# Performance work log

Hardware: AMD Instinct MI355X
Metric: run time of the kernel (lower is better)

The kernel has to match this reference:

```python
import jax, jax.numpy as jnp
import numpy as np

TEMP = 0.1
QUEUE_SIZE = 512
CUTOFF_KM = 25.0
EARTH_R_KM = 6371.0088


def _normalize(x, eps=1e-12):
    # F.normalize: x / max(||x||, eps)
    n = jnp.linalg.norm(x, axis=-1, keepdims=True)
    return x / jnp.maximum(n, eps)


def _haversine_km(g1, g2):
    # g1: (B,2) [lat,lon] degrees; g2: (S,2) -> (B,S) great-circle km
    r = jnp.pi / 180.0
    lat1 = g1[:, 0:1] * r
    lon1 = g1[:, 1:2] * r
    lat2 = g2[None, :, 0] * r
    lon2 = g2[None, :, 1] * r
    dlat = lat2 - lat1
    dlon = lon2 - lon1
    a = jnp.sin(dlat / 2) ** 2 + jnp.cos(lat1) * jnp.cos(lat2) * jnp.sin(dlon / 2) ** 2
    return 2.0 * EARTH_R_KM * jnp.arcsin(jnp.sqrt(jnp.clip(a, 0.0, 1.0)))


def setup_inputs() -> dict:
    key = jax.random.key(0)
    k = jax.random.split(key, 7)
    n_aug, B, D, S = 4, 256, 768, 65536
    V = jax.random.normal(k[0], (n_aug, B, D), jnp.float32)
    L = jax.random.normal(k[1], (B, D), jnp.float32)
    gps = jnp.concatenate([
        jax.random.uniform(k[2], (B, 1), jnp.float32, -90.0, 90.0),
        jax.random.uniform(k[3], (B, 1), jnp.float32, -180.0, 180.0)], axis=1)
    support_features = jax.random.normal(k[4], (S, D), jnp.float32)
    support_gps = jnp.concatenate([
        jax.random.uniform(k[5], (S, 1), jnp.float32, -90.0, 90.0),
        jax.random.uniform(k[6], (S, 1), jnp.float32, -180.0, 180.0)], axis=1)
    return {"V": V, "L": L, "gps": gps,
            "support_features": support_features, "support_gps": support_gps}


def reference(V, L, gps, support_features, support_gps):
    # org joint embedding always from V[0]; nearest neighbour over raw support feats
    org = _normalize(V[0] * L)                                   # (B,D)
    sim = org @ support_features.T                               # (B,S)
    nn_idx = jnp.argmax(sim, axis=1)                             # (B,)
    nn = _normalize(support_features[nn_idx])                    # (B,D)

    # augmented joints for j = 1..n_aug-1
    augs = _normalize(V[1:] * L[None])                           # (J,B,D)
    # numerator always uses V[1] (as in the original code), constant over j
    num = jnp.einsum('bd,bd->b', nn, augs[0]) / TEMP             # (B,)

    # in-batch denominator: sum_i exp(nn_b . aug_{j,i} / T)
    batch_den = jnp.exp(jnp.einsum('bd,jid->jbi', nn, augs) / TEMP).sum(axis=2)  # (J,B)

    # GPS-filtered negative queue: first QUEUE_SIZE support entries > 25 km away,
    # zero-padded (zero rows contribute exp(0) = 1, matching the torch code)
    mask = _haversine_km(gps, support_gps) > CUTOFF_KM           # (B,S)
    order = jnp.argsort(jnp.where(mask, 0, 1), axis=1)[:, :QUEUE_SIZE]  # stable: kept in original order
    valid = jnp.take_along_axis(mask, order, axis=1)             # (B,Q)
    qfeat = support_features[order] * valid[..., None]           # (B,Q,D)
    queue_den = jnp.exp(jnp.einsum('bd,bqd->bq', nn, qfeat) / TEMP).sum(axis=1)  # (B,)

    den = jnp.log(batch_den + queue_den[None, :])                # (J,B)
    loss = -(num[None, :] - den).sum() / V.shape[1]
    return loss
```

## Files before the change

### kernel.cpp

```cpp
#include <hip/hip_runtime.h>
#include <hip/hip_bf16.h>

#define B_ROWS 256
#define S_SUP  65536
#define D_DIM  768
#define QSZ    512
#define NCHUNK 12
#define CHUNK_BYTES 32768

typedef short bf16x8 __attribute__((ext_vector_type(8)));
typedef float f32x4  __attribute__((ext_vector_type(4)));

__device__ __forceinline__ bf16x8 cvt8(float4 a, float4 b) {
  bf16x8 r;
  r[0] = (short)(__float_as_uint(a.x) >> 16);
  r[1] = (short)(__float_as_uint(a.y) >> 16);
  r[2] = (short)(__float_as_uint(a.z) >> 16);
  r[3] = (short)(__float_as_uint(a.w) >> 16);
  r[4] = (short)(__float_as_uint(b.x) >> 16);
  r[5] = (short)(__float_as_uint(b.y) >> 16);
  r[6] = (short)(__float_as_uint(b.z) >> 16);
  r[7] = (short)(__float_as_uint(b.w) >> 16);
  return r;
}

__device__ __forceinline__ void gl_lds16(const void* g, void* l) {
  __builtin_amdgcn_global_load_lds(
      (const __attribute__((address_space(1))) unsigned int*)g,
      (__attribute__((address_space(3))) unsigned int*)l, 16, 0, 0);
}

__device__ __forceinline__ float block_sum(float v) {
  __shared__ float tmp[4];
  #pragma unroll
  for (int m = 32; m >= 1; m >>= 1) v += __shfl_xor(v, m, 64);
  __syncthreads();
  if ((threadIdx.x & 63) == 0) tmp[threadIdx.x >> 6] = v;
  __syncthreads();
  return tmp[0] + tmp[1] + tmp[2] + tmp[3];
}

__device__ __forceinline__ double block_sum_d(double v) {
  __shared__ double tmp[4];
  #pragma unroll
  for (int m = 32; m >= 1; m >>= 1) v += __shfl_xor(v, m, 64);
  __syncthreads();
  if ((threadIdx.x & 63) == 0) tmp[threadIdx.x >> 6] = v;
  __syncthreads();
  return tmp[0] + tmp[1] + tmp[2] + tmp[3];
}

__global__ __launch_bounds__(256) void init_kernel(unsigned long long* gmax, double* bden) {
  int t = threadIdx.x;
  gmax[t] = 0ull;
  for (int i = t; i < 3 * B_ROWS; i += 256) bden[i] = 0.0;
}

__global__ __launch_bounds__(256) void prep_kernel(const float* __restrict__ V,
                                                   const float* __restrict__ L,
                                                   unsigned short* __restrict__ orgb,
                                                   float* __restrict__ augs) {
  int jb = blockIdx.x;
  int j = jb >> 8, b = jb & 255;
  int tid = threadIdx.x;
  const float* v = V + ((size_t)j * B_ROWS + b) * D_DIM;
  const float* l = L + (size_t)b * D_DIM;
  float p[3]; float ssq = 0.f;
  #pragma unroll
  for (int i = 0; i < 3; ++i) {
    int k = tid + 256 * i;
    p[i] = v[k] * l[k];
    ssq += p[i] * p[i];
  }
  ssq = block_sum(ssq);
  float inv = 1.0f / fmaxf(sqrtf(ssq), 1e-12f);
  if (j == 0) {
    #pragma unroll
    for (int i = 0; i < 3; ++i) {
      int k = tid + 256 * i;
      unsigned short hv = (unsigned short)(__float_as_uint(p[i] * inv) >> 16);
      int c = k >> 6, kk = k & 63, jg = kk >> 3, e = kk & 7;
      orgb[c * 16384 + b * 64 + ((jg ^ (b & 7)) << 3) + e] = hv;
    }
  } else {
    float* dst = augs + ((size_t)(j - 1) * B_ROWS + b) * D_DIM;
    #pragma unroll
    for (int i = 0; i < 3; ++i) dst[tid + 256 * i] = p[i] * inv;
  }
}

__global__ __launch_bounds__(256) void sim_argmax_kernel(const unsigned short* __restrict__ orgb,
                                                         const float* __restrict__ sf,
                                                         unsigned long long* __restrict__ gmax) {
  const int tid  = threadIdx.x;
  const int w    = tid >> 6;
  const int lid  = tid & 63;
  const int quad = lid >> 4;
  const int r15  = lid & 15;
  const int s_col = blockIdx.x * 64 + w * 16 + r15;

  __shared__ __align__(16) char smem[CHUNK_BYTES];

  f32x4 acc[16];
  #pragma unroll
  for (int t = 0; t < 16; ++t) acc[t] = (f32x4){0.f, 0.f, 0.f, 0.f};

  const float* bp = sf + (size_t)s_col * D_DIM + quad * 8;
  const char* gsrc_base = (const char*)orgb;

  for (int c = 0; c < NCHUNK; ++c) {
    {
      const char* g = gsrc_base + c * CHUNK_BYTES + w * 8192 + lid * 16;
      char* ldst = smem + w * 8192;
      #pragma unroll
      for (int i = 0; i < 8; ++i)
        gl_lds16(g + i * 1024, ldst + i * 1024);
    }
    __syncthreads();

    #pragma unroll
    for (int k1 = 0; k1 < 2; ++k1) {
      int k0 = c * 64 + k1 * 32;
      float4 b0 = *(const float4*)(bp + k0);
      float4 b1 = *(const float4*)(bp + k0 + 4);
      bf16x8 bf = cvt8(b0, b1);
      int abase = r15 * 128 + (((k1 * 4 + quad) ^ (r15 & 7)) << 4);
      #pragma unroll
      for (int t = 0; t < 16; ++t) {
        bf16x8 af = *(const bf16x8*)(smem + abase + t * 2048);
        acc[t] = __builtin_amdgcn_mfma_f32_16x16x32_bf16(af, bf, acc[t], 0, 0, 0);
      }
    }
    __syncthreads();
  }

  __shared__ float smax[4 * 256];
  __shared__ int   sidx[4 * 256];
  #pragma unroll
  for (int t = 0; t < 16; ++t) {
    #pragma unroll
    for (int r = 0; r < 4; ++r) {
      float v = acc[t][r];
      int   idx = s_col;
      #pragma unroll
      for (int m = 1; m < 16; m <<= 1) {
        float ov = __shfl_xor(v, m, 64);
        int   oi = __shfl_xor(idx, m, 64);
        if (ov > v || (ov == v && oi < idx)) { v = ov; idx = oi; }
      }
      if (r15 == 0) {
        int b = 16 * t + 4 * quad + r;
        smax[w * 256 + b] = v;
        sidx[w * 256 + b] = idx;
      }
    }
  }
  __syncthreads();
  {
    int b = tid;
    float v = smax[b]; int idx = sidx[b];
    #pragma unroll
    for (int w2 = 1; w2 < 4; ++w2) {
      float ov = smax[w2 * 256 + b]; int oi = sidx[w2 * 256 + b];
      if (ov > v || (ov == v && oi < idx)) { v = ov; idx = oi; }
    }
    unsigned u = __float_as_uint(v);
    unsigned key = (u & 0x80000000u) ? ~u : (u | 0x80000000u);
    unsigned long long packed = ((unsigned long long)key << 32) |
                                (unsigned long long)(0xFFFFFFFFu - (unsigned)idx);
    atomicMax(gmax + b, packed);
  }
}

__global__ __launch_bounds__(256) void nn_kernel(const unsigned long long* __restrict__ gmax,
                                                 const float* __restrict__ sf,
                                                 const float* __restrict__ augs,
                                                 float* __restrict__ nn,
                                                 float* __restrict__ nnT,
                                                 float* __restrict__ num) {
  int b = blockIdx.x, tid = threadIdx.x;
  int idx = (int)(0xFFFFFFFFu - (unsigned)(gmax[b] & 0xFFFFFFFFull));
  const float* row = sf + (size_t)idx * D_DIM;
  float p[3]; float ssq = 0.f;
  #pragma unroll
  for (int i = 0; i < 3; ++i) { p[i] = row[tid + 256 * i]; ssq += p[i] * p[i]; }
  ssq = block_sum(ssq);
  float inv = 1.0f / fmaxf(sqrtf(ssq), 1e-12f);
  const float* a0 = augs + (size_t)b * D_DIM;
  float dot = 0.f;
  #pragma unroll
  for (int i = 0; i < 3; ++i) {
    int k = tid + 256 * i;
    float nv = p[i] * inv;
    nn[(size_t)b * D_DIM + k] = nv;
    nnT[(size_t)k * B_ROWS + b] = nv;
    dot += nv * a0[k];
  }
  dot = block_sum(dot);
  if (tid == 0) num[b] = dot * 10.0f;
}

__global__ __launch_bounds__(256) void bden_kernel(const float* __restrict__ augs,
                                                   const float* __restrict__ nnT,
                                                   double* __restrict__ bden) {
  int jc = blockIdx.x;
  int j = jc >> 6, c = jc & 63;
  int i0 = c * 4;
  __shared__ float s_aug[4 * D_DIM];
  const float* src = augs + ((size_t)j * B_ROWS + i0) * D_DIM;
  for (int idx = threadIdx.x; idx < 4 * D_DIM; idx += 256) s_aug[idx] = src[idx];
  __syncthreads();
  int b = threadIdx.x;
  float a0 = 0.f, a1 = 0.f, a2 = 0.f, a3 = 0.f;
  for (int k = 0; k < D_DIM; ++k) {
    float nv = nnT[(size_t)k * B_ROWS + b];
    a0 += nv * s_aug[k];
    a1 += nv * s_aug[D_DIM + k];
    a2 += nv * s_aug[2 * D_DIM + k];
    a3 += nv * s_aug[3 * D_DIM + k];
  }
  double v = exp((double)a0 * 10.0) + exp((double)a1 * 10.0) +
             exp((double)a2 * 10.0) + exp((double)a3 * 10.0);
  atomicAdd(&bden[j * B_ROWS + b], v);
}

__global__ __launch_bounds__(256) void queue_kernel(const float* __restrict__ gps,
                                                    const float* __restrict__ sgps,
                                                    const float* __restrict__ sf,
                                                    const float* __restrict__ nn,
                                                    double* __restrict__ qden) {
  int b = blockIdx.x, tid = threadIdx.x;
  int w = tid >> 6, lane = tid & 63;
  __shared__ int qidx[QSZ];
  __shared__ int s_count;
  __shared__ int s_wcnt[4];
  __shared__ __align__(16) float s_nn[D_DIM];
  __shared__ double s_gsum[16];
  for (int k = tid; k < D_DIM; k += 256) s_nn[k] = nn[(size_t)b * D_DIM + k];
  if (tid == 0) s_count = 0;
  __syncthreads();

  const float r = 0.017453292519943295f;
  float lat1 = gps[b * 2 + 0] * r, lon1 = gps[b * 2 + 1] * r;
  float cl1 = cosf(lat1);
  int base = 0;
  while (true) {
    int count = s_count;
    if (count >= QSZ || base >= S_SUP) break;
    int s = base + tid;
    float lat2 = sgps[s * 2 + 0] * r, lon2 = sgps[s * 2 + 1] * r;
    float sdlat = sinf((lat2 - lat1) * 0.5f);
    float sdlon = sinf((lon2 - lon1) * 0.5f);
    float a = sdlat * sdlat + cl1 * cosf(lat2) * sdlon * sdlon;
    a = fminf(fmaxf(a, 0.f), 1.f);
    float d = 2.0f * 6371.0088f * asinf(sqrtf(a));
    bool valid = d > 25.0f;

    unsigned long long m = __ballot(valid);
    int wc = __popcll(m);
    if (lane == 0) s_wcnt[w] = wc;
    __syncthreads();
    int wbase = count;
    for (int i = 0; i < w; ++i) wbase += s_wcnt[i];
    int pos = wbase + __popcll(m & ((1ull << lane) - 1ull));
    if (valid && pos < QSZ) qidx[pos] = s;
    __syncthreads();
    if (tid == 0) {
      int total = s_wcnt[0] + s_wcnt[1] + s_wcnt[2] + s_wcnt[3];
      s_count = min(QSZ, count + total);
    }
    base += 256;
    __syncthreads();
  }
  int count = s_count;

  int g  = lane >> 4;
  int l2 = lane & 15;
  double acc = 0.0;
  const float4* nn4 = (const float4*)s_nn;
  for (int q = w * 4 + g; q < count; q += 16) {
    const float4* row = (const float4*)(sf + (size_t)qidx[q] * D_DIM);
    float dot = 0.f;
    #pragma unroll
    for (int i = 0; i < 12; ++i) {
      float4 a = row[l2 + 16 * i];
      float4 nv = nn4[l2 + 16 * i];
      dot += a.x * nv.x + a.y * nv.y + a.z * nv.z + a.w * nv.w;
    }
    #pragma unroll
    for (int m2 = 8; m2 >= 1; m2 >>= 1) dot += __shfl_xor(dot, m2, 16);
    if (l2 == 0) acc += exp((double)dot * 10.0);
  }
  if (l2 == 0) s_gsum[w * 4 + g] = acc;
  __syncthreads();
  if (tid == 0) {
    double t = (double)(QSZ - count);
    #pragma unroll
    for (int i = 0; i < 16; ++i) t += s_gsum[i];
    qden[b] = t;
  }
}

__global__ __launch_bounds__(256) void loss_kernel(const float* __restrict__ num,
                                                   const double* __restrict__ bden,
                                                   const double* __restrict__ qden,
                                                   float* __restrict__ out) {
  int b = threadIdx.x;
  double q = qden[b];
  double n = (double)num[b];
  double t = 0.0;
  #pragma unroll
  for (int j = 0; j < 3; ++j) t += n - log(bden[j * B_ROWS + b] + q);
  t = block_sum_d(t);
  if (b == 0) out[0] = (float)(-t / 256.0);
}

extern "C" void kernel_launch(void* const* d_in, const int* in_sizes, int n_in,
                              void* d_out, int out_size, void* d_ws, size_t ws_size,
                              hipStream_t stream) {
  const float* V    = (const float*)d_in[0];
  const float* L    = (const float*)d_in[1];
  const float* gps  = (const float*)d_in[2];
  const float* sf   = (const float*)d_in[3];
  const float* sgps = (const float*)d_in[4];
  float* out = (float*)d_out;

  char* ws = (char*)d_ws;
  size_t off = 0;
  unsigned short* orgb = (unsigned short*)(ws + off); off += 393216;
  float* augs = (float*)(ws + off); off += 2359296;
  float* nn   = (float*)(ws + off); off += 786432;
  float* nnT  = (float*)(ws + off); off += 786432;
  float* num  = (float*)(ws + off); off += 1024;
  double* bden = (double*)(ws + off); off += 6144;
  double* qden = (double*)(ws + off); off += 2048;
  unsigned long long* gmax = (unsigned long long*)(ws + off); off += 2048;

  init_kernel<<<1, 256, 0, stream>>>(gmax, bden);
  prep_kernel<<<1024, 256, 0, stream>>>(V, L, orgb, augs);
  sim_argmax_kernel<<<S_SUP / 64, 256, 0, stream>>>(orgb, sf, gmax);
  nn_kernel<<<B_ROWS, 256, 0, stream>>>(gmax, sf, augs, nn, nnT, num);
  bden_kernel<<<192, 256, 0, stream>>>(augs, nnT, bden);
  queue_kernel<<<B_ROWS, 256, 0, stream>>>(gps, sgps, sf, nn, qden);
  loss_kernel<<<1, 256, 0, stream>>>(num, bden, qden, out);
}
```

Measured before the change: 432.3 us.

## Double-buffer sim GEMM with LDS-staged B tiles and fuse small kernels

Restructures the similarity/argmax kernel. Each wave now computes a 64x64 register tile (4x4 MFMA tiles) instead of 16x256. The support-feature B operand is converted to bf16 once into LDS and shared across waves, and A and B chunks are double-buffered so the next loads overlap the current MFMAs. The argmax epilogue does atomicMax per row directly, dropping the shared-memory cross-wave reduction. It also folds the init work into prep_kernel and merges nn_kernel with queue_kernel, which removes the intermediate nn buffer and two launches, at the cost of more LDS per block and more atomics.

```diff
diff --git a/kernel.cpp b/kernel.cpp
--- a/kernel.cpp
+++ b/kernel.cpp
@@ -6,7 +6,8 @@
 #define D_DIM  768
 #define QSZ    512
 #define NCHUNK 12
-#define CHUNK_BYTES 32768
+#define ACH_BYTES 32768
+#define BCH_BYTES 8192
 
 typedef short bf16x8 __attribute__((ext_vector_type(8)));
 typedef float f32x4  __attribute__((ext_vector_type(4)));
@@ -50,19 +51,19 @@
   return tmp[0] + tmp[1] + tmp[2] + tmp[3];
 }
 
-__global__ __launch_bounds__(256) void init_kernel(unsigned long long* gmax, double* bden) {
-  int t = threadIdx.x;
-  gmax[t] = 0ull;
-  for (int i = t; i < 3 * B_ROWS; i += 256) bden[i] = 0.0;
-}
-
 __global__ __launch_bounds__(256) void prep_kernel(const float* __restrict__ V,
                                                    const float* __restrict__ L,
                                                    unsigned short* __restrict__ orgb,
-                                                   float* __restrict__ augs) {
+                                                   float* __restrict__ augs,
+                                                   unsigned long long* __restrict__ gmax,
+                                                   double* __restrict__ bden) {
   int jb = blockIdx.x;
   int j = jb >> 8, b = jb & 255;
   int tid = threadIdx.x;
+  if (jb == 0) {
+    gmax[tid] = 0ull;
+    for (int i = tid; i < 3 * B_ROWS; i += 256) bden[i] = 0.0;
+  }
   const float* v = V + ((size_t)j * B_ROWS + b) * D_DIM;
   const float* l = L + (size_t)b * D_DIM;
   float p[3]; float ssq = 0.f;
@@ -89,59 +90,90 @@
   }
 }
 
-__global__ __launch_bounds__(256) void sim_argmax_kernel(const unsigned short* __restrict__ orgb,
-                                                         const float* __restrict__ sf,
-                                                         unsigned long long* __restrict__ gmax) {
+__global__ __launch_bounds__(256, 2) void sim_argmax_kernel(const unsigned short* __restrict__ orgb,
+                                                            const float* __restrict__ sf,
+                                                            unsigned long long* __restrict__ gmax) {
   const int tid  = threadIdx.x;
   const int w    = tid >> 6;
   const int lid  = tid & 63;
   const int quad = lid >> 4;
   const int r15  = lid & 15;
-  const int s_col = blockIdx.x * 64 + w * 16 + r15;
-
-  __shared__ __align__(16) char smem[CHUNK_BYTES];
-
-  f32x4 acc[16];
-  #pragma unroll
-  for (int t = 0; t < 16; ++t) acc[t] = (f32x4){0.f, 0.f, 0.f, 0.f};
-
-  const float* bp = sf + (size_t)s_col * D_DIM + quad * 8;
-  const char* gsrc_base = (const char*)orgb;
+  const int s0   = blockIdx.x * 64;
+
+  __shared__ __align__(16) char bufA[2][ACH_BYTES];
+  __shared__ __align__(16) char bufB[2][BCH_BYTES];
+
+  f32x4 acc[4][4];
+  #pragma unroll
+  for (int mt = 0; mt < 4; ++mt)
+    #pragma unroll
+    for (int nt = 0; nt < 4; ++nt) acc[mt][nt] = (f32x4){0.f, 0.f, 0.f, 0.f};
+
+  const float* bsrc = sf + (size_t)(s0 + lid) * D_DIM + w * 16;
+  const char*  asrc = (const char*)orgb;
+  const int lrow = lid * 128;
+  const int sl0  = (((2 * w)     ^ (lid & 7)) << 4);
+  const int sl1  = (((2 * w + 1) ^ (lid & 7)) << 4);
+
+  {
+    const char* g = asrc + w * 8192 + lid * 16;
+    char* l = bufA[0] + w * 8192;
+    #pragma unroll
+    for (int i = 0; i < 8; ++i) gl_lds16(g + i * 1024, l + i * 1024);
+    const float4* bp = (const float4*)bsrc;
+    float4 q0 = bp[0], q1 = bp[1], q2 = bp[2], q3 = bp[3];
+    *(bf16x8*)(bufB[0] + lrow + sl0) = cvt8(q0, q1);
+    *(bf16x8*)(bufB[0] + lrow + sl1) = cvt8(q2, q3);
+  }
+  __syncthreads();
 
   for (int c = 0; c < NCHUNK; ++c) {
-    {
-      const char* g = gsrc_base + c * CHUNK_BYTES + w * 8192 + lid * 16;
-      char* ldst = smem + w * 8192;
-      #pragma unroll
-      for (int i = 0; i < 8; ++i)
-        gl_lds16(g + i * 1024, ldst + i * 1024);
-    }
-    __syncthreads();
-
+    float4 q0, q1, q2, q3;
+    const int nb = (c + 1) & 1;
+    if (c < NCHUNK - 1) {
+      const char* g = asrc + (c + 1) * ACH_BYTES + w * 8192 + lid * 16;
+      char* l = bufA[nb] + w * 8192;
+      #pragma unroll
+      for (int i = 0; i < 8; ++i) gl_lds16(g + i * 1024, l + i * 1024);
+      const float4* bp = (const float4*)(bsrc + (c + 1) * 64);
+      q0 = bp[0]; q1 = bp[1]; q2 = bp[2]; q3 = bp[3];
+    }
+    const char* Ac = bufA[c & 1];
+    const char* Bc = bufB[c & 1];
     #pragma unroll
     for (int k1 = 0; k1 < 2; ++k1) {
-      int k0 = c * 64 + k1 * 32;
-      float4 b0 = *(const float4*)(bp + k0);
-      float4 b1 = *(const float4*)(bp + k0 + 4);
-      bf16x8 bf = cvt8(b0, b1);
-      int abase = r15 * 128 + (((k1 * 4 + quad) ^ (r15 & 7)) << 4);
-      #pragma unroll
-      for (int t = 0; t < 16; ++t) {
-        bf16x8 af = *(const bf16x8*)(smem + abase + t * 2048);
-        acc[t] = __builtin_amdgcn_mfma_f32_16x16x32_bf16(af, bf, acc[t], 0, 0, 0);
+      const int slot = (((k1 * 4 + quad) ^ (r15 & 7)) << 4);
+      bf16x8 af[4], bfr[4];
+      #pragma unroll
+      for (int mt = 0; mt < 4; ++mt)
+        af[mt] = *(const bf16x8*)(Ac + (64 * w + 16 * mt + r15) * 128 + slot);
+      #pragma unroll
+      for (int nt = 0; nt < 4; ++nt)
+        bfr[nt] = *(const bf16x8*)(Bc + (16 * nt + r15) * 128 + slot);
+      #pragma unroll
+      for (int mt = 0; mt < 4; ++mt)
+        #pragma unroll
+        for (int nt = 0; nt < 4; ++nt)
+          acc[mt][nt] = __builtin_amdgcn_mfma_f32_16x16x32_bf16(af[mt], bfr[nt], acc[mt][nt], 0, 0, 0);
+    }
+    if (c < NCHUNK - 1) {
+      *(bf16x8*)(bufB[nb] + lrow + sl0) = cvt8(q0, q1);
+      *(bf16x8*)(bufB[nb] + lrow + sl1) = cvt8(q2, q3);
+      __syncthreads();
+    }
+  }
+
+  #pragma unroll
+  for (int mt = 0; mt < 4; ++mt) {
+    #pragma unroll
+    for (int r = 0; r < 4; ++r) {
+      float v = acc[mt][0][r];
+      int idx = s0 + r15;
+      #pragma unroll
+      for (int nt = 1; nt < 4; ++nt) {
+        float c2 = acc[mt][nt][r];
+        if (c2 > v) { v = c2; idx = s0 + nt * 16 + r15; }
       }
-    }
-    __syncthreads();
-  }
-
-  __shared__ float smax[4 * 256];
-  __shared__ int   sidx[4 * 256];
-  #pragma unroll
-  for (int t = 0; t < 16; ++t) {
-    #pragma unroll
-    for (int r = 0; r < 4; ++r) {
-      float v = acc[t][r];
-      int   idx = s_col;
       #pragma unroll
       for (int m = 1; m < 16; m <<= 1) {
         float ov = __shfl_xor(v, m, 64);
@@ -149,36 +181,33 @@
         if (ov > v || (ov == v && oi < idx)) { v = ov; idx = oi; }
       }
       if (r15 == 0) {
-        int b = 16 * t + 4 * quad + r;
-        smax[w * 256 + b] = v;
-        sidx[w * 256 + b] = idx;
+        int mg = 64 * w + 16 * mt + 4 * quad + r;
+        unsigned u = __float_as_uint(v);
+        unsigned key = (u & 0x80000000u) ? ~u : (u | 0x80000000u);
+        unsigned long long packed = ((unsigned long long)key << 32) |
+                                    (unsigned long long)(0xFFFFFFFFu - (unsigned)idx);
+        atomicMax(gmax + mg, packed);
       }
     }
   }
-  __syncthreads();
-  {
-    int b = tid;
-    float v = smax[b]; int idx = sidx[b];
-    #pragma unroll
-    for (int w2 = 1; w2 < 4; ++w2) {
-      float ov = smax[w2 * 256 + b]; int oi = sidx[w2 * 256 + b];
-      if (ov > v || (ov == v && oi < idx)) { v = ov; idx = oi; }
-    }
-    unsigned u = __float_as_uint(v);
-    unsigned key = (u & 0x80000000u) ? ~u : (u | 0x80000000u);
-    unsigned long long packed = ((unsigned long long)key << 32) |
-                                (unsigned long long)(0xFFFFFFFFu - (unsigned)idx);
-    atomicMax(gmax + b, packed);
-  }
-}
-
-__global__ __launch_bounds__(256) void nn_kernel(const unsigned long long* __restrict__ gmax,
-                                                 const float* __restrict__ sf,
-                                                 const float* __restrict__ augs,
-                                                 float* __restrict__ nn,
-                                                 float* __restrict__ nnT,
-                                                 float* __restrict__ num) {
+}
+
+__global__ __launch_bounds__(256) void nnqueue_kernel(const unsigned long long* __restrict__ gmax,
+                                                      const float* __restrict__ sf,
+                                                      const float* __restrict__ augs,
+                                                      const float* __restrict__ gps,
+                                                      const float* __restrict__ sgps,
+                                                      float* __restrict__ nnT,
+                                                      float* __restrict__ num,
+                                                      double* __restrict__ qden) {
   int b = blockIdx.x, tid = threadIdx.x;
+  int w = tid >> 6, lane = tid & 63;
+  __shared__ __align__(16) float s_nn[D_DIM];
+  __shared__ int qidx[QSZ];
+  __shared__ int s_count;
+  __shared__ int s_wcnt[4];
+  __shared__ double s_gsum[16];
+
   int idx = (int)(0xFFFFFFFFu - (unsigned)(gmax[b] & 0xFFFFFFFFull));
   const float* row = sf + (size_t)idx * D_DIM;
   float p[3]; float ssq = 0.f;
@@ -192,52 +221,12 @@
   for (int i = 0; i < 3; ++i) {
     int k = tid + 256 * i;
     float nv = p[i] * inv;
-    nn[(size_t)b * D_DIM + k] = nv;
+    s_nn[k] = nv;
     nnT[(size_t)k * B_ROWS + b] = nv;
     dot += nv * a0[k];
   }
   dot = block_sum(dot);
-  if (tid == 0) num[b] = dot * 10.0f;
-}
-
-__global__ __launch_bounds__(256) void bden_kernel(const float* __restrict__ augs,
-                                                   const float* __restrict__ nnT,
-                                                   double* __restrict__ bden) {
-  int jc = blockIdx.x;
-  int j = jc >> 6, c = jc & 63;
-  int i0 = c * 4;
-  __shared__ float s_aug[4 * D_DIM];
-  const float* src = augs + ((size_t)j * B_ROWS + i0) * D_DIM;
-  for (int idx = threadIdx.x; idx < 4 * D_DIM; idx += 256) s_aug[idx] = src[idx];
-  __syncthreads();
-  int b = threadIdx.x;
-  float a0 = 0.f, a1 = 0.f, a2 = 0.f, a3 = 0.f;
-  for (int k = 0; k < D_DIM; ++k) {
-    float nv = nnT[(size_t)k * B_ROWS + b];
-    a0 += nv * s_aug[k];
-    a1 += nv * s_aug[D_DIM + k];
-    a2 += nv * s_aug[2 * D_DIM + k];
-    a3 += nv * s_aug[3 * D_DIM + k];
-  }
-  double v = exp((double)a0 * 10.0) + exp((double)a1 * 10.0) +
-             exp((double)a2 * 10.0) + exp((double)a3 * 10.0);
-  atomicAdd(&bden[j * B_ROWS + b], v);
-}
-
-__global__ __launch_bounds__(256) void queue_kernel(const float* __restrict__ gps,
-                                                    const float* __restrict__ sgps,
-                                                    const float* __restrict__ sf,
-                                                    const float* __restrict__ nn,
-                                                    double* __restrict__ qden) {
-  int b = blockIdx.x, tid = threadIdx.x;
-  int w = tid >> 6, lane = tid & 63;
-  __shared__ int qidx[QSZ];
-  __shared__ int s_count;
-  __shared__ int s_wcnt[4];
-  __shared__ __align__(16) float s_nn[D_DIM];
-  __shared__ double s_gsum[16];
-  for (int k = tid; k < D_DIM; k += 256) s_nn[k] = nn[(size_t)b * D_DIM + k];
-  if (tid == 0) s_count = 0;
+  if (tid == 0) { num[b] = dot * 10.0f; s_count = 0; }
   __syncthreads();
 
   const float r = 0.017453292519943295f;
@@ -279,17 +268,17 @@
   double acc = 0.0;
   const float4* nn4 = (const float4*)s_nn;
   for (int q = w * 4 + g; q < count; q += 16) {
-    const float4* row = (const float4*)(sf + (size_t)qidx[q] * D_DIM);
-    float dot = 0.f;
+    const float4* rr = (const float4*)(sf + (size_t)qidx[q] * D_DIM);
+    float d2 = 0.f;
     #pragma unroll
     for (int i = 0; i < 12; ++i) {
-      float4 a = row[l2 + 16 * i];
+      float4 a = rr[l2 + 16 * i];
       float4 nv = nn4[l2 + 16 * i];
-      dot += a.x * nv.x + a.y * nv.y + a.z * nv.z + a.w * nv.w;
-    }
-    #pragma unroll
-    for (int m2 = 8; m2 >= 1; m2 >>= 1) dot += __shfl_xor(dot, m2, 16);
-    if (l2 == 0) acc += exp((double)dot * 10.0);
+      d2 += a.x * nv.x + a.y * nv.y + a.z * nv.z + a.w * nv.w;
+    }
+    #pragma unroll
+    for (int m2 = 8; m2 >= 1; m2 >>= 1) d2 += __shfl_xor(d2, m2, 16);
+    if (l2 == 0) acc += exp((double)d2 * 10.0);
   }
   if (l2 == 0) s_gsum[w * 4 + g] = acc;
   __syncthreads();
@@ -299,6 +288,30 @@
     for (int i = 0; i < 16; ++i) t += s_gsum[i];
     qden[b] = t;
   }
+}
+
+__global__ __launch_bounds__(256) void bden_kernel(const float* __restrict__ augs,
+                                                   const float* __restrict__ nnT,
+                                                   double* __restrict__ bden) {
+  int jc = blockIdx.x;
+  int j = jc >> 6, c = jc & 63;
+  int i0 = c * 4;
+  __shared__ float s_aug[4 * D_DIM];
+  const float* src = augs + ((size_t)j * B_ROWS + i0) * D_DIM;
+  for (int idx = threadIdx.x; idx < 4 * D_DIM; idx += 256) s_aug[idx] = src[idx];
+  __syncthreads();
+  int b = threadIdx.x;
+  float a0 = 0.f, a1 = 0.f, a2 = 0.f, a3 = 0.f;
+  for (int k = 0; k < D_DIM; ++k) {
+    float nv = nnT[(size_t)k * B_ROWS + b];
+    a0 += nv * s_aug[k];
+    a1 += nv * s_aug[D_DIM + k];
+    a2 += nv * s_aug[2 * D_DIM + k];
+    a3 += nv * s_aug[3 * D_DIM + k];
+  }
+  double v = exp((double)a0 * 10.0) + exp((double)a1 * 10.0) +
+             exp((double)a2 * 10.0) + exp((double)a3 * 10.0);
+  atomicAdd(&bden[j * B_ROWS + b], v);
 }
 
 __global__ __launch_bounds__(256) void loss_kernel(const float* __restrict__ num,
@@ -329,18 +342,15 @@
   size_t off = 0;
   unsigned short* orgb = (unsigned short*)(ws + off); off += 393216;
   float* augs = (float*)(ws + off); off += 2359296;
-  float* nn   = (float*)(ws + off); off += 786432;
   float* nnT  = (float*)(ws + off); off += 786432;
   float* num  = (float*)(ws + off); off += 1024;
   double* bden = (double*)(ws + off); off += 6144;
   double* qden = (double*)(ws + off); off += 2048;
   unsigned long long* gmax = (unsigned long long*)(ws + off); off += 2048;
 
-  init_kernel<<<1, 256, 0, stream>>>(gmax, bden);
-  prep_kernel<<<1024, 256, 0, stream>>>(V, L, orgb, augs);
+  prep_kernel<<<1024, 256, 0, stream>>>(V, L, orgb, augs, gmax, bden);
   sim_argmax_kernel<<<S_SUP / 64, 256, 0, stream>>>(orgb, sf, gmax);
-  nn_kernel<<<B_ROWS, 256, 0, stream>>>(gmax, sf, augs, nn, nnT, num);
+  nnqueue_kernel<<<B_ROWS, 256, 0, stream>>>(gmax, sf, augs, gps, sgps, nnT, num, qden);
   bden_kernel<<<192, 256, 0, stream>>>(augs, nnT, bden);
-  queue_kernel<<<B_ROWS, 256, 0, stream>>>(gps, sgps, sf, nn, qden);
   loss_kernel<<<1, 256, 0, stream>>>(num, bden, qden, out);
 }
```

Result: no change. 436.2 us (+0.9%).
